# Optimization experiments

Measured on AMD Instinct MI355X. Metric: run time of the kernel, lower is better.

The kernel has to match this reference:

```python
import jax, jax.numpy as jnp
import numpy as np

BIG_NUM = 1000000000.0

def setup_inputs() -> dict:
    key0 = jax.random.key(0)
    k1, k2, k3, k4 = jax.random.split(key0, 4)
    B, T, D = 64, 4096, 512
    query = jax.random.normal(k1, (B, D), dtype=jnp.float32)
    key = jax.random.normal(k2, (B, T, D), dtype=jnp.float32)
    value = jax.random.normal(k3, (B, T, D), dtype=jnp.float32)
    mask = jax.random.randint(k4, (B, T), 0, 2, dtype=jnp.int32)
    return {"query": query, "key": key, "value": value, "mask": mask}

def reference(query, key, value, mask):
    # query: [B, D], key/value: [B, T, D], mask: [B, T] (1 = keep, 0 = mask)
    D = query.shape[1]
    scale = D ** 0.5
    # energy[b, t] = key[b, t, :] . query[b, :]
    energy = jnp.einsum('btd,bd->bt', key, query) / scale
    energy = energy + (mask.astype(jnp.float32) - 1.0) * BIG_NUM
    attn = jax.nn.softmax(energy, axis=-1)          # [B, T]
    context = jnp.einsum('bt,btd->bd', attn, value)  # [B, D]
    return (context, attn)
```

## Files before the change

kernel.cpp:

```cpp
#include <hip/hip_runtime.h>
#include <math.h>

#define B 64
#define T 4096
#define D 512
#define NCH 32
#define CHT (T / NCH)
#define WSTRIP 32

__device__ __forceinline__ float wave_sum64(float v) {
#pragma unroll
    for (int off = 32; off; off >>= 1)
        v += __shfl_xor(v, off, 64);
    return v;
}

__global__ __launch_bounds__(256) void energy_exp_kernel(const float* __restrict__ q,
                                                         const float* __restrict__ k,
                                                         const int* __restrict__ mask,
                                                         float* __restrict__ attn,
                                                         float* __restrict__ chunk_sums) {
    const float INV_SCALE = 0.04419417382415922f;

    __shared__ int sm_list[4][WSTRIP];
    __shared__ float sred[4];

    int blk = blockIdx.x;
    int b = blk >> 5;
    int ch = blk & 31;
    int wave = threadIdx.x >> 6;
    int lane = threadIdx.x & 63;

    const float* qb = q + b * D;
    float4 qa = *(const float4*)(qb + lane * 4);
    float4 qc = *(const float4*)(qb + 256 + lane * 4);

    int t0 = ch * CHT + wave * WSTRIP;
    const float* kbase = k + ((size_t)b * T + t0) * D;

    int mv = (lane < WSTRIP) ? mask[b * T + t0 + lane] : 0;
    unsigned int mbits = (unsigned int)__ballot(mv != 0);
    int cnt = __popc(mbits);
    if (lane < WSTRIP) {
        if (mv != 0) {
            int pre = __popc(mbits & ((1u << lane) - 1u));
            sm_list[wave][pre] = lane;
        } else {
            attn[(size_t)b * T + t0 + lane] = 0.0f;
        }
    }

    int r3 = ((lane >> 5) & 1) | (((lane >> 4) & 1) << 1) | (((lane >> 3) & 1) << 2);
    float gsum = 0.f;
    int ngrp = (cnt + 7) >> 3;

#pragma unroll 1
    for (int g = 0; g < ngrp; ++g) {
        float d8[8];
#pragma unroll
        for (int rr = 0; rr < 8; ++rr) {
            int slot = g * 8 + rr;
            int row = sm_list[wave][slot < cnt ? slot : 0];
            const float* kr = kbase + (size_t)row * D;
            float4 ka = *(const float4*)(kr + lane * 4);
            float4 kc = *(const float4*)(kr + 256 + lane * 4);
            d8[rr] = ka.x * qa.x + ka.y * qa.y + ka.z * qa.z + ka.w * qa.w
                   + kc.x * qc.x + kc.y * qc.y + kc.z * qc.z + kc.w * qc.w;
        }
        bool b5 = (lane & 32) != 0;
        float e[4];
#pragma unroll
        for (int i = 0; i < 4; ++i) {
            float u = b5 ? d8[2*i+1] : d8[2*i];
            float s = b5 ? d8[2*i]   : d8[2*i+1];
            e[i] = u + __shfl_xor(s, 32, 64);
        }
        bool b4 = (lane & 16) != 0;
        float f[2];
#pragma unroll
        for (int i = 0; i < 2; ++i) {
            float u = b4 ? e[2*i+1] : e[2*i];
            float s = b4 ? e[2*i]   : e[2*i+1];
            f[i] = u + __shfl_xor(s, 16, 64);
        }
        bool b3 = (lane & 8) != 0;
        float u = b3 ? f[1] : f[0];
        float s = b3 ? f[0] : f[1];
        float h = u + __shfl_xor(s, 8, 64);
        h += __shfl_xor(h, 4, 64);
        h += __shfl_xor(h, 2, 64);
        h += __shfl_xor(h, 1, 64);

        int slot = g * 8 + r3;
        float gval = 0.f;
        if (slot < cnt) {
            gval = __expf(h * INV_SCALE);
            if ((lane & 7) == 0) {
                int row = sm_list[wave][slot];
                attn[(size_t)b * T + t0 + row] = gval;
            }
        }
        gsum += gval;
    }

    float ws = wave_sum64(gsum) * 0.125f;
    if (lane == 0) sred[wave] = ws;
    __syncthreads();
    if (threadIdx.x == 0)
        chunk_sums[blk] = (sred[0] + sred[1]) + (sred[2] + sred[3]);
}

__global__ __launch_bounds__(256) void context_partial_kernel(float* __restrict__ attn,
                                                              const float* __restrict__ v,
                                                              const float* __restrict__ chunk_sums,
                                                              float* __restrict__ partial) {
    __shared__ float sa[CHT];
    __shared__ int   sm_c[4][64];
    __shared__ float sm_a[4][64];

    int blk = blockIdx.x;
    int b = blk >> 5;
    int ch = blk & 31;
    int tid = threadIdx.x;
    int wave = tid >> 6;
    int lane = tid & 63;

    float cs = (lane < NCH) ? chunk_sums[b * NCH + lane] : 0.f;
    float denom = wave_sum64(cs);
    float inv = 1.0f / denom;

    if (tid < CHT) sa[tid] = attn[(size_t)b * T + ch * CHT + tid];
    __syncthreads();

    int par = wave >> 1;
    int dcol = ((wave & 1) * 64 + lane) * 4;

    int myrow = 2 * lane + par;
    float mya0 = sa[myrow];
    unsigned long long ball = __ballot(mya0 != 0.0f);
    int cnt = __popcll(ball);
    int pre = __popcll(ball & ((1ull << lane) - 1ull));
    if (mya0 != 0.0f) {
        sm_c[wave][pre] = myrow;
        sm_a[wave][pre] = mya0;
    }
    __syncthreads();

    int  crow = sm_c[wave][lane];
    float ca  = sm_a[wave][lane];

    const float* vb = v + ((size_t)b * T + ch * CHT) * D + dcol;

    float4 acc = {0.f, 0.f, 0.f, 0.f};
#pragma unroll 8
    for (int j = 0; j < cnt; ++j) {
        int row = __shfl(crow, j, 64);
        float a = __shfl(ca, j, 64);
        float4 vv = *(const float4*)(vb + (size_t)row * D);
        acc.x += a * vv.x; acc.y += a * vv.y;
        acc.z += a * vv.z; acc.w += a * vv.w;
    }
    acc.x *= inv; acc.y *= inv; acc.z *= inv; acc.w *= inv;
    *(float4*)(partial + ((size_t)(b * 64 + ch * 2 + par)) * D + dcol) = acc;

    if (tid < CHT)
        attn[(size_t)b * T + ch * CHT + tid] = sa[tid] * inv;
}

__global__ __launch_bounds__(256) void context_reduce_kernel(const float* __restrict__ partial,
                                                             float* __restrict__ ctx) {
    int b = blockIdx.x;
    int tid = threadIdx.x;
    int d0 = tid * 2;
    float2 acc = {0.f, 0.f};
#pragma unroll 8
    for (int j = 0; j < 64; ++j) {
        float2 p = *(const float2*)(partial + ((size_t)(b * 64 + j)) * D + d0);
        acc.x += p.x;
        acc.y += p.y;
    }
    *(float2*)(ctx + (size_t)b * D + d0) = acc;
}

extern "C" void kernel_launch(void* const* d_in, const int* in_sizes, int n_in,
                              void* d_out, int out_size, void* d_ws, size_t ws_size,
                              hipStream_t stream) {
    const float* q    = (const float*)d_in[0];
    const float* k    = (const float*)d_in[1];
    const float* v    = (const float*)d_in[2];
    const int*   mask = (const int*)d_in[3];

    float* ctx  = (float*)d_out;
    float* attn = (float*)d_out + B * D;

    float* chunk_sums = (float*)d_ws;
    float* partial    = (float*)d_ws + 8192;

    energy_exp_kernel<<<B * NCH, 256, 0, stream>>>(q, k, mask, attn, chunk_sums);
    context_partial_kernel<<<B * NCH, 256, 0, stream>>>(attn, v, chunk_sums, partial);
    context_reduce_kernel<<<B, 256, 0, stream>>>(partial, ctx);
}
```

Before: 117.5 us.

## Stage V rows into LDS with async global_load_lds double buffering

Rewrites the context partial kernel so nonzero-attention V rows are compacted into one list per chunk and streamed into a double-buffered LDS area with global_load_lds, eight rows per batch. Each thread then accumulates two columns from LDS, which replaces the earlier split of each chunk's rows by parity across wave pairs. This halves the number of partial rows the reduce kernel reads and aims to overlap V loads with compute. The cost is extra barriers and LDS traffic, and manual vmcnt waits that depend on the exact number of outstanding loads per wave.

```diff
diff --git a/kernel.cpp b/kernel.cpp
--- a/kernel.cpp
+++ b/kernel.cpp
@@ -7,12 +7,24 @@
 #define NCH 32
 #define CHT (T / NCH)
 #define WSTRIP 32
+#define VBATCH 8
+
+typedef __attribute__((address_space(1))) const void global_cv;
+typedef __attribute__((address_space(3))) void lds_v;
 
 __device__ __forceinline__ float wave_sum64(float v) {
 #pragma unroll
     for (int off = 32; off; off >>= 1)
         v += __shfl_xor(v, off, 64);
     return v;
+}
+
+__device__ __forceinline__ void stage_row(const float* __restrict__ gsrc_row,
+                                          float* lds_row, int lane) {
+    __builtin_amdgcn_global_load_lds((global_cv*)(gsrc_row + lane * 4),
+                                     (lds_v*)(lds_row), 16, 0, 0);
+    __builtin_amdgcn_global_load_lds((global_cv*)(gsrc_row + 256 + lane * 4),
+                                     (lds_v*)(lds_row + 256), 16, 0, 0);
 }
 
 __global__ __launch_bounds__(256) void energy_exp_kernel(const float* __restrict__ q,
@@ -114,9 +126,11 @@
                                                               const float* __restrict__ v,
                                                               const float* __restrict__ chunk_sums,
                                                               float* __restrict__ partial) {
-    __shared__ float sa[CHT];
-    __shared__ int   sm_c[4][64];
-    __shared__ float sm_a[4][64];
+    __shared__ __align__(16) float vbuf[2][VBATCH][D];
+    __shared__ float sa_raw[CHT];
+    __shared__ int   rows[CHT + VBATCH];
+    __shared__ float avals[CHT + VBATCH];
+    __shared__ int   scnt;
 
     int blk = blockIdx.x;
     int b = blk >> 5;
@@ -129,42 +143,80 @@
     float denom = wave_sum64(cs);
     float inv = 1.0f / denom;
 
-    if (tid < CHT) sa[tid] = attn[(size_t)b * T + ch * CHT + tid];
+    if (tid < CHT) sa_raw[tid] = attn[(size_t)b * T + ch * CHT + tid];
     __syncthreads();
 
-    int par = wave >> 1;
-    int dcol = ((wave & 1) * 64 + lane) * 4;
-
-    int myrow = 2 * lane + par;
-    float mya0 = sa[myrow];
-    unsigned long long ball = __ballot(mya0 != 0.0f);
-    int cnt = __popcll(ball);
-    int pre = __popcll(ball & ((1ull << lane) - 1ull));
-    if (mya0 != 0.0f) {
-        sm_c[wave][pre] = myrow;
-        sm_a[wave][pre] = mya0;
+    if (wave == 0) {
+        float a0 = sa_raw[lane];
+        unsigned long long bl0 = __ballot(a0 != 0.0f);
+        int c0 = __popcll(bl0);
+        if (a0 != 0.0f) {
+            int p = __popcll(bl0 & ((1ull << lane) - 1ull));
+            rows[p] = lane; avals[p] = a0;
+        }
+        float a1 = sa_raw[64 + lane];
+        unsigned long long bl1 = __ballot(a1 != 0.0f);
+        int c1 = __popcll(bl1);
+        if (a1 != 0.0f) {
+            int p = c0 + __popcll(bl1 & ((1ull << lane) - 1ull));
+            rows[p] = 64 + lane; avals[p] = a1;
+        }
+        int cnt = c0 + c1;
+        if (lane < VBATCH) {
+            int safe0 = (cnt > 0) ? rows[0] : 0;
+            rows[cnt + lane] = safe0;
+            avals[cnt + lane] = 0.0f;
+        }
+        if (lane == 0) scnt = cnt;
     }
     __syncthreads();
 
-    int  crow = sm_c[wave][lane];
-    float ca  = sm_a[wave][lane];
-
-    const float* vb = v + ((size_t)b * T + ch * CHT) * D + dcol;
-
-    float4 acc = {0.f, 0.f, 0.f, 0.f};
-#pragma unroll 8
-    for (int j = 0; j < cnt; ++j) {
-        int row = __shfl(crow, j, 64);
-        float a = __shfl(ca, j, 64);
-        float4 vv = *(const float4*)(vb + (size_t)row * D);
-        acc.x += a * vv.x; acc.y += a * vv.y;
-        acc.z += a * vv.z; acc.w += a * vv.w;
-    }
-    acc.x *= inv; acc.y *= inv; acc.z *= inv; acc.w *= inv;
-    *(float4*)(partial + ((size_t)(b * 64 + ch * 2 + par)) * D + dcol) = acc;
+    int cnt = scnt;
+    int nb = (cnt + VBATCH - 1) / VBATCH;
+    const float* vchunk = v + ((size_t)b * T + ch * CHT) * D;
+
+    if (nb > 0) {
+        int s0 = wave * 2;
+        stage_row(vchunk + (size_t)rows[s0] * D,     &vbuf[0][wave * 2][0],     lane);
+        stage_row(vchunk + (size_t)rows[s0 + 1] * D, &vbuf[0][wave * 2 + 1][0], lane);
+    }
+    if (nb > 1) {
+        int s0 = VBATCH + wave * 2;
+        stage_row(vchunk + (size_t)rows[s0] * D,     &vbuf[1][wave * 2][0],     lane);
+        stage_row(vchunk + (size_t)rows[s0 + 1] * D, &vbuf[1][wave * 2 + 1][0], lane);
+    }
+
+    float2 acc = {0.f, 0.f};
+    int c0 = tid * 2;
+#pragma unroll 1
+    for (int i = 0; i < nb; ++i) {
+        if (i + 1 < nb) asm volatile("s_waitcnt vmcnt(4)" ::: "memory");
+        else            asm volatile("s_waitcnt vmcnt(0)" ::: "memory");
+        __builtin_amdgcn_s_barrier();
+
+        const float (*buf)[D] = vbuf[i & 1];
+        int base = i * VBATCH;
+#pragma unroll
+        for (int r = 0; r < VBATCH; ++r) {
+            float a = avals[base + r];
+            float2 vv = *(const float2*)&buf[r][c0];
+            acc.x += a * vv.x;
+            acc.y += a * vv.y;
+        }
+        __builtin_amdgcn_s_barrier();
+
+        if (i + 2 < nb) {
+            int s0 = (i + 2) * VBATCH + wave * 2;
+            stage_row(vchunk + (size_t)rows[s0] * D,     &vbuf[i & 1][wave * 2][0],     lane);
+            stage_row(vchunk + (size_t)rows[s0 + 1] * D, &vbuf[i & 1][wave * 2 + 1][0], lane);
+        }
+    }
+
+    acc.x *= inv; acc.y *= inv;
+    *(float2*)(partial + (size_t)(b * NCH + ch) * D + c0) = acc;
 
     if (tid < CHT)
-        attn[(size_t)b * T + ch * CHT + tid] = sa[tid] * inv;
+        attn[(size_t)b * T + ch * CHT + tid] = sa_raw[tid] * inv;
 }
 
 __global__ __launch_bounds__(256) void context_reduce_kernel(const float* __restrict__ partial,
@@ -174,8 +226,8 @@
     int d0 = tid * 2;
     float2 acc = {0.f, 0.f};
 #pragma unroll 8
-    for (int j = 0; j < 64; ++j) {
-        float2 p = *(const float2*)(partial + ((size_t)(b * 64 + j)) * D + d0);
+    for (int j = 0; j < NCH; ++j) {
+        float2 p = *(const float2*)(partial + (size_t)(b * NCH + j) * D + d0);
         acc.x += p.x;
         acc.y += p.y;
     }
```

Result: faster. 112.9 us (-3.9%).

## Fuse energy and context passes with double-buffered LDS staging of K/V rows

Applied to the files above, without the earlier changes.

Merges the energy/exp kernel and the context-partial kernel into one kernel that loads each unmasked K and V row once. Rows are staged into LDS with global_load_lds in a two-deep double buffer, using explicit vmcnt waits. The context is accumulated unnormalized per wave, and a small finalize kernel then applies the softmax denominator to both context and attn. This removes a kernel launch, the attn round-trip and the serialized second pass over V. In exchange it uses heavy LDS (about 72KB per block), which may cut occupancy, and it relies on hand-written waitcnt ordering. Only two rows are in flight per wave.

```diff
diff --git a/kernel.cpp b/kernel.cpp
--- a/kernel.cpp
+++ b/kernel.cpp
@@ -7,6 +7,10 @@
 #define NCH 32
 #define CHT (T / NCH)
 #define WSTRIP 32
+#define KB2 2
+
+typedef __attribute__((address_space(1))) const void global_cv;
+typedef __attribute__((address_space(3))) void lds_v;
 
 __device__ __forceinline__ float wave_sum64(float v) {
 #pragma unroll
@@ -15,15 +19,27 @@
     return v;
 }
 
-__global__ __launch_bounds__(256) void energy_exp_kernel(const float* __restrict__ q,
+__device__ __forceinline__ void stage_row(const float* __restrict__ gsrc_row,
+                                          float* lds_row, int lane) {
+    __builtin_amdgcn_global_load_lds((global_cv*)(gsrc_row + lane * 4),
+                                     (lds_v*)(lds_row), 16, 0, 0);
+    __builtin_amdgcn_global_load_lds((global_cv*)(gsrc_row + 256 + lane * 4),
+                                     (lds_v*)(lds_row + 256), 16, 0, 0);
+}
+
+__global__ __launch_bounds__(256) void fused_attn_kernel(const float* __restrict__ q,
                                                          const float* __restrict__ k,
+                                                         const float* __restrict__ v,
                                                          const int* __restrict__ mask,
                                                          float* __restrict__ attn,
-                                                         float* __restrict__ chunk_sums) {
+                                                         float* __restrict__ chunk_sums,
+                                                         float* __restrict__ partial) {
     const float INV_SCALE = 0.04419417382415922f;
 
-    __shared__ int sm_list[4][WSTRIP];
+    __shared__ __align__(16) float kvbuf[2][4][KB2][2][D];
+    __shared__ int sm_list[4][WSTRIP + KB2];
     __shared__ float sred[4];
+    __shared__ float sacc[4][D];
 
     int blk = blockIdx.x;
     int b = blk >> 5;
@@ -37,10 +53,12 @@
 
     int t0 = ch * CHT + wave * WSTRIP;
     const float* kbase = k + ((size_t)b * T + t0) * D;
+    const float* vbase = v + ((size_t)b * T + t0) * D;
 
     int mv = (lane < WSTRIP) ? mask[b * T + t0 + lane] : 0;
     unsigned int mbits = (unsigned int)__ballot(mv != 0);
     int cnt = __popc(mbits);
+    int row0 = (cnt > 0) ? (__ffs(mbits) - 1) : 0;
     if (lane < WSTRIP) {
         if (mv != 0) {
             int pre = __popc(mbits & ((1u << lane) - 1u));
@@ -49,137 +67,136 @@
             attn[(size_t)b * T + t0 + lane] = 0.0f;
         }
     }
-
-    int r3 = ((lane >> 5) & 1) | (((lane >> 4) & 1) << 1) | (((lane >> 3) & 1) << 2);
+    if (lane < KB2) sm_list[wave][cnt + lane] = row0;
+
+    int ngrp = (cnt + KB2 - 1) >> 1;
+
+    if (ngrp > 0) {
+#pragma unroll
+        for (int r = 0; r < KB2; ++r) {
+            int row = sm_list[wave][r];
+            stage_row(kbase + (size_t)row * D, &kvbuf[0][wave][r][0][0], lane);
+            stage_row(vbase + (size_t)row * D, &kvbuf[0][wave][r][1][0], lane);
+        }
+    }
+    if (ngrp > 1) {
+#pragma unroll
+        for (int r = 0; r < KB2; ++r) {
+            int row = sm_list[wave][KB2 + r];
+            stage_row(kbase + (size_t)row * D, &kvbuf[1][wave][r][0][0], lane);
+            stage_row(vbase + (size_t)row * D, &kvbuf[1][wave][r][1][0], lane);
+        }
+    }
+
     float gsum = 0.f;
-    int ngrp = (cnt + 7) >> 3;
+    float4 accA = {0.f, 0.f, 0.f, 0.f}, accC = {0.f, 0.f, 0.f, 0.f};
+    int rown = lane >> 5;
 
 #pragma unroll 1
-    for (int g = 0; g < ngrp; ++g) {
-        float d8[8];
-#pragma unroll
-        for (int rr = 0; rr < 8; ++rr) {
-            int slot = g * 8 + rr;
-            int row = sm_list[wave][slot < cnt ? slot : 0];
-            const float* kr = kbase + (size_t)row * D;
-            float4 ka = *(const float4*)(kr + lane * 4);
-            float4 kc = *(const float4*)(kr + 256 + lane * 4);
-            d8[rr] = ka.x * qa.x + ka.y * qa.y + ka.z * qa.z + ka.w * qa.w
+    for (int i = 0; i < ngrp; ++i) {
+        if (i + 1 < ngrp) asm volatile("s_waitcnt vmcnt(8)" ::: "memory");
+        else              asm volatile("s_waitcnt vmcnt(0)" ::: "memory");
+
+        float d2[KB2];
+        float4 va[KB2], vc[KB2];
+#pragma unroll
+        for (int rr = 0; rr < KB2; ++rr) {
+            float4 ka = *(const float4*)&kvbuf[i & 1][wave][rr][0][lane * 4];
+            float4 kc = *(const float4*)&kvbuf[i & 1][wave][rr][0][256 + lane * 4];
+            d2[rr] = ka.x * qa.x + ka.y * qa.y + ka.z * qa.z + ka.w * qa.w
                    + kc.x * qc.x + kc.y * qc.y + kc.z * qc.z + kc.w * qc.w;
-        }
+            va[rr] = *(const float4*)&kvbuf[i & 1][wave][rr][1][lane * 4];
+            vc[rr] = *(const float4*)&kvbuf[i & 1][wave][rr][1][256 + lane * 4];
+        }
+
         bool b5 = (lane & 32) != 0;
-        float e[4];
-#pragma unroll
-        for (int i = 0; i < 4; ++i) {
-            float u = b5 ? d8[2*i+1] : d8[2*i];
-            float s = b5 ? d8[2*i]   : d8[2*i+1];
-            e[i] = u + __shfl_xor(s, 32, 64);
-        }
-        bool b4 = (lane & 16) != 0;
-        float f[2];
-#pragma unroll
-        for (int i = 0; i < 2; ++i) {
-            float u = b4 ? e[2*i+1] : e[2*i];
-            float s = b4 ? e[2*i]   : e[2*i+1];
-            f[i] = u + __shfl_xor(s, 16, 64);
-        }
-        bool b3 = (lane & 8) != 0;
-        float u = b3 ? f[1] : f[0];
-        float s = b3 ? f[0] : f[1];
-        float h = u + __shfl_xor(s, 8, 64);
+        float u = b5 ? d2[1] : d2[0];
+        float s = b5 ? d2[0] : d2[1];
+        float h = u + __shfl_xor(s, 32, 64);
+        h += __shfl_xor(h, 16, 64);
+        h += __shfl_xor(h, 8, 64);
         h += __shfl_xor(h, 4, 64);
         h += __shfl_xor(h, 2, 64);
         h += __shfl_xor(h, 1, 64);
 
-        int slot = g * 8 + r3;
+        int slot = i * KB2 + rown;
         float gval = 0.f;
         if (slot < cnt) {
             gval = __expf(h * INV_SCALE);
-            if ((lane & 7) == 0) {
-                int row = sm_list[wave][slot];
-                attn[(size_t)b * T + t0 + row] = gval;
+            if ((lane & 31) == 0)
+                attn[(size_t)b * T + t0 + sm_list[wave][slot]] = gval;
+        }
+        gsum += gval;
+
+        asm volatile("s_waitcnt lgkmcnt(0)" ::: "memory");
+        if (i + 2 < ngrp) {
+            int s0 = (i + 2) * KB2;
+#pragma unroll
+            for (int r = 0; r < KB2; ++r) {
+                int row = sm_list[wave][s0 + r];
+                stage_row(kbase + (size_t)row * D, &kvbuf[i & 1][wave][r][0][0], lane);
+                stage_row(vbase + (size_t)row * D, &kvbuf[i & 1][wave][r][1][0], lane);
             }
         }
-        gsum += gval;
-    }
-
-    float ws = wave_sum64(gsum) * 0.125f;
+
+        float g0 = __shfl(gval, 0, 64);
+        float g1 = __shfl(gval, 32, 64);
+        accA.x += g0 * va[0].x; accA.y += g0 * va[0].y;
+        accA.z += g0 * va[0].z; accA.w += g0 * va[0].w;
+        accC.x += g0 * vc[0].x; accC.y += g0 * vc[0].y;
+        accC.z += g0 * vc[0].z; accC.w += g0 * vc[0].w;
+        accA.x += g1 * va[1].x; accA.y += g1 * va[1].y;
+        accA.z += g1 * va[1].z; accA.w += g1 * va[1].w;
+        accC.x += g1 * vc[1].x; accC.y += g1 * vc[1].y;
+        accC.z += g1 * vc[1].z; accC.w += g1 * vc[1].w;
+    }
+
+    *(float4*)(&sacc[wave][lane * 4]) = accA;
+    *(float4*)(&sacc[wave][256 + lane * 4]) = accC;
+    float ws = wave_sum64(gsum) * 0.03125f;
     if (lane == 0) sred[wave] = ws;
     __syncthreads();
+
+    int c0 = threadIdx.x * 2;
+    float2 p;
+    p.x = (sacc[0][c0]     + sacc[1][c0])     + (sacc[2][c0]     + sacc[3][c0]);
+    p.y = (sacc[0][c0 + 1] + sacc[1][c0 + 1]) + (sacc[2][c0 + 1] + sacc[3][c0 + 1]);
+    *(float2*)(partial + (size_t)(b * NCH + ch) * D + c0) = p;
+
     if (threadIdx.x == 0)
         chunk_sums[blk] = (sred[0] + sred[1]) + (sred[2] + sred[3]);
 }
 
-__global__ __launch_bounds__(256) void context_partial_kernel(float* __restrict__ attn,
-                                                              const float* __restrict__ v,
-                                                              const float* __restrict__ chunk_sums,
-                                                              float* __restrict__ partial) {
-    __shared__ float sa[CHT];
-    __shared__ int   sm_c[4][64];
-    __shared__ float sm_a[4][64];
-
-    int blk = blockIdx.x;
-    int b = blk >> 5;
-    int ch = blk & 31;
+__global__ __launch_bounds__(256) void finalize_kernel(const float* __restrict__ partial,
+                                                       const float* __restrict__ chunk_sums,
+                                                       float* __restrict__ attn,
+                                                       float* __restrict__ ctx) {
+    int b = blockIdx.x;
     int tid = threadIdx.x;
-    int wave = tid >> 6;
     int lane = tid & 63;
 
     float cs = (lane < NCH) ? chunk_sums[b * NCH + lane] : 0.f;
     float denom = wave_sum64(cs);
     float inv = 1.0f / denom;
 
-    if (tid < CHT) sa[tid] = attn[(size_t)b * T + ch * CHT + tid];
-    __syncthreads();
-
-    int par = wave >> 1;
-    int dcol = ((wave & 1) * 64 + lane) * 4;
-
-    int myrow = 2 * lane + par;
-    float mya0 = sa[myrow];
-    unsigned long long ball = __ballot(mya0 != 0.0f);
-    int cnt = __popcll(ball);
-    int pre = __popcll(ball & ((1ull << lane) - 1ull));
-    if (mya0 != 0.0f) {
-        sm_c[wave][pre] = myrow;
-        sm_a[wave][pre] = mya0;
-    }
-    __syncthreads();
-
-    int  crow = sm_c[wave][lane];
-    float ca  = sm_a[wave][lane];
-
-    const float* vb = v + ((size_t)b * T + ch * CHT) * D + dcol;
-
-    float4 acc = {0.f, 0.f, 0.f, 0.f};
-#pragma unroll 8
-    for (int j = 0; j < cnt; ++j) {
-        int row = __shfl(crow, j, 64);
-        float a = __shfl(ca, j, 64);
-        float4 vv = *(const float4*)(vb + (size_t)row * D);
-        acc.x += a * vv.x; acc.y += a * vv.y;
-        acc.z += a * vv.z; acc.w += a * vv.w;
-    }
-    acc.x *= inv; acc.y *= inv; acc.z *= inv; acc.w *= inv;
-    *(float4*)(partial + ((size_t)(b * 64 + ch * 2 + par)) * D + dcol) = acc;
-
-    if (tid < CHT)
-        attn[(size_t)b * T + ch * CHT + tid] = sa[tid] * inv;
-}
-
-__global__ __launch_bounds__(256) void context_reduce_kernel(const float* __restrict__ partial,
-                                                             float* __restrict__ ctx) {
-    int b = blockIdx.x;
-    int tid = threadIdx.x;
-    int d0 = tid * 2;
+    int c = tid * 2;
     float2 acc = {0.f, 0.f};
 #pragma unroll 8
-    for (int j = 0; j < 64; ++j) {
-        float2 p = *(const float2*)(partial + ((size_t)(b * 64 + j)) * D + d0);
+    for (int j = 0; j < NCH; ++j) {
+        float2 p = *(const float2*)(partial + (size_t)(b * NCH + j) * D + c);
         acc.x += p.x;
         acc.y += p.y;
     }
-    *(float2*)(ctx + (size_t)b * D + d0) = acc;
+    acc.x *= inv; acc.y *= inv;
+    *(float2*)(ctx + (size_t)b * D + c) = acc;
+
+#pragma unroll
+    for (int j = 0; j < 4; ++j) {
+        size_t idx = (size_t)b * T + (size_t)j * 1024 + tid * 4;
+        float4 x = *(const float4*)(attn + idx);
+        x.x *= inv; x.y *= inv; x.z *= inv; x.w *= inv;
+        *(float4*)(attn + idx) = x;
+    }
 }
 
 extern "C" void kernel_launch(void* const* d_in, const int* in_sizes, int n_in,
@@ -196,7 +213,6 @@
     float* chunk_sums = (float*)d_ws;
     float* partial    = (float*)d_ws + 8192;
 
-    energy_exp_kernel<<<B * NCH, 256, 0, stream>>>(q, k, mask, attn, chunk_sums);
-    context_partial_kernel<<<B * NCH, 256, 0, stream>>>(attn, v, chunk_sums, partial);
-    context_reduce_kernel<<<B, 256, 0, stream>>>(partial, ctx);
-}
+    fused_attn_kernel<<<B * NCH, 256, 0, stream>>>(q, k, v, mask, attn, chunk_sums, partial);
+    finalize_kernel<<<B, 256, 0, stream>>>(partial, chunk_sums, attn, ctx);
+}
```

Measured after the change: 114.1 us. 1.03x faster.
